# Performance work log

Hardware: AMD Instinct MI355X
Metric: run time of the kernel (lower is better)

The kernel has to match this reference:

```python
import jax, jax.numpy as jnp
import numpy as np

N, D, IN, OUT, K = 50000, 16, 256, 128, 4  # nodes, sampled degree, input_size, output_size, heads
LEAKY_SLOPE = 0.01  # torch F.leaky_relu default


def setup_inputs() -> dict:
    key = jax.random.key(0)
    k1, k2, k3, k4 = jax.random.split(key, 4)
    X = jax.random.normal(k1, (N, IN), dtype=jnp.float32)
    W = jax.random.normal(k2, (K, OUT, IN), dtype=jnp.float32) * 0.05
    a = jax.random.normal(k3, (K, 2 * OUT), dtype=jnp.float32) * 0.05
    neighbor_idx = jax.random.randint(k4, (N, D), 0, N)  # fixed-degree neighbor sample
    return {"X": X, "W": W, "a": a, "neighbor_idx": neighbor_idx}


def reference(X, W, a, neighbor_idx):
    # X: [N, IN]; W: [K, OUT, IN]; a: [K, 2*OUT]; neighbor_idx: [N, D]
    out_dim = W.shape[1]
    # Per-head linear map of every node once: Wh[k, n] = W[k] @ X[n]
    Wh = jnp.einsum('koi,ni->kno', W, X)                       # [K, N, OUT]
    # a splits: first OUT weights multiply mapped neighbour, second OUT multiply mapped self
    a_nb, a_self = a[:, :out_dim], a[:, out_dim:]
    e_nb = jnp.einsum('kno,ko->kn', Wh, a_nb)                  # [K, N] score contribution as a neighbour
    e_self = jnp.einsum('kno,ko->kn', Wh, a_self)              # [K, N] score contribution as center node
    # Edge logits: e[k, i, d] = leaky_relu(a_nb.Wh[j] + a_self.Wh[i]), j = neighbor_idx[i, d]
    e = jax.nn.leaky_relu(e_nb[:, neighbor_idx] + e_self[:, :, None], LEAKY_SLOPE)  # [K, N, D]
    alpha = jax.nn.softmax(e, axis=-1)                         # softmax over each node's neighbour set
    Wh_nb = jnp.take(Wh, neighbor_idx, axis=1)                 # [K, N, D, OUT] gathered neighbour features
    h = jnp.einsum('knd,kndo->kno', alpha, Wh_nb)              # [K, N, OUT] attention-weighted aggregate
    # Concatenate heads along feature dim, matching per-node head-concat in the torch loop
    return jnp.transpose(h, (1, 0, 2)).reshape(X.shape[0], -1)  # [N, K*OUT]
```

## Files before the change

### kernel.cpp

```cpp
#include <hip/hip_runtime.h>

#define N_NODES 50000
#define D_NB 16
#define IN_DIM 256
#define OUT_DIM 128
#define K_HEADS 4
#define SLOPE 0.01f
#define NSLICE 16
#define SLICE_COLS 32

typedef __attribute__((ext_vector_type(8))) short short8;
typedef __attribute__((ext_vector_type(4))) float f32x4;

static __device__ __forceinline__ unsigned f2bf(float f) {
    unsigned u = __float_as_uint(f);
    unsigned r = u + 0x7fffu + ((u >> 16) & 1u);
    return r >> 16;
}
static __device__ __forceinline__ float bf2f(unsigned short b) {
    return __uint_as_float(((unsigned)b) << 16);
}

__global__ void wb_kernel(const float* __restrict__ W, unsigned short* __restrict__ Wb) {
    int id = blockIdx.x * blockDim.x + threadIdx.x;
    if (id < K_HEADS * OUT_DIM * IN_DIM) Wb[id] = (unsigned short)f2bf(W[id]);
}

__global__ __launch_bounds__(256) void wt8_kernel(
    const float* __restrict__ W, const float* __restrict__ a, float* __restrict__ wt8)
{
    const int i = threadIdx.x;
    #pragma unroll
    for (int k = 0; k < K_HEADS; ++k) {
        float s0 = 0.f, s1 = 0.f;
        for (int o = 0; o < OUT_DIM; ++o) {
            const float w = W[((size_t)k * OUT_DIM + o) * IN_DIM + i];
            s0 += w * a[k * 2 * OUT_DIM + o];
            s1 += w * a[k * 2 * OUT_DIM + OUT_DIM + o];
        }
        wt8[(k * 2 + 0) * IN_DIM + i] = s0;
        wt8[(k * 2 + 1) * IN_DIM + i] = s1;
    }
}

__global__ __launch_bounds__(256) void prep_kernel(
    const float* __restrict__ X, const float* __restrict__ wt8,
    unsigned short* __restrict__ Xb, float* __restrict__ e_nb, float* __restrict__ e_self)
{
    const int t = threadIdx.x;
    const int w = t >> 6;
    const int lane = t & 63;
    const int n = blockIdx.x * 4 + w;

    const float4 x = *(const float4*)(X + (size_t)n * IN_DIM + lane * 4);
    uint2 pk;
    pk.x = f2bf(x.x) | (f2bf(x.y) << 16);
    pk.y = f2bf(x.z) | (f2bf(x.w) << 16);
    *(uint2*)(Xb + (size_t)n * IN_DIM + lane * 4) = pk;

    float p[8];
    #pragma unroll
    for (int v = 0; v < 8; ++v) {
        const float4 wv = *(const float4*)(wt8 + v * IN_DIM + lane * 4);
        p[v] = x.x * wv.x + x.y * wv.y + x.z * wv.z + x.w * wv.w;
    }
    #pragma unroll
    for (int sh = 32; sh >= 1; sh >>= 1) {
        #pragma unroll
        for (int v = 0; v < 8; ++v) p[v] += __shfl_xor(p[v], sh);
    }
    if (lane < 8) {
        const int k = lane >> 1;
        float* dst = (lane & 1) ? e_self : e_nb;
        dst[(size_t)k * N_NODES + n] = p[lane];
    }
}

__global__ __launch_bounds__(256) void agg_kernel(
    const int* __restrict__ nidx, const unsigned short* __restrict__ Xb,
    const float* __restrict__ e_nb, const float* __restrict__ e_self,
    unsigned short* __restrict__ aggX, int n0, int nc)
{
    const int t = threadIdx.x;
    const int w = t >> 6;
    const int lane = t & 63;
    const int n = n0 + blockIdx.x * 4 + w;
    if (n >= n0 + nc || n >= N_NODES) return;

    const int k = lane >> 4;
    const int dl = lane & 15;

    const int nbr = nidx[(size_t)n * D_NB + dl];
    const float x = e_nb[(size_t)k * N_NODES + nbr] + e_self[(size_t)k * N_NODES + n];
    const float v = x > 0.f ? x : SLOPE * x;
    float m = v;
    #pragma unroll
    for (int sh = 8; sh >= 1; sh >>= 1) m = fmaxf(m, __shfl_xor(m, sh, 16));
    const float pz = __expf(v - m);
    float sum = pz;
    #pragma unroll
    for (int sh = 8; sh >= 1; sh >>= 1) sum += __shfl_xor(sum, sh, 16);
    const float alpha = pz / sum;

    float acc[4][4] = {};
    #pragma unroll
    for (int h = 0; h < 2; ++h) {
        uint2 u[8];
        #pragma unroll
        for (int b = 0; b < 8; ++b) {
            const int nd = __shfl(nbr, h * 8 + b);
            u[b] = *(const uint2*)(Xb + (size_t)nd * IN_DIM + lane * 4);
        }
        #pragma unroll
        for (int b = 0; b < 8; ++b) {
            const float x0 = bf2f((unsigned short)(u[b].x & 0xffffu));
            const float x1 = bf2f((unsigned short)(u[b].x >> 16));
            const float x2 = bf2f((unsigned short)(u[b].y & 0xffffu));
            const float x3 = bf2f((unsigned short)(u[b].y >> 16));
            #pragma unroll
            for (int kk = 0; kk < 4; ++kk) {
                const float ad = __shfl(alpha, kk * 16 + h * 8 + b);
                acc[kk][0] += ad * x0;
                acc[kk][1] += ad * x1;
                acc[kk][2] += ad * x2;
                acc[kk][3] += ad * x3;
            }
        }
    }
    #pragma unroll
    for (int kk = 0; kk < 4; ++kk) {
        uint2 pk;
        pk.x = f2bf(acc[kk][0]) | (f2bf(acc[kk][1]) << 16);
        pk.y = f2bf(acc[kk][2]) | (f2bf(acc[kk][3]) << 16);
        *(uint2*)(aggX + ((size_t)kk * nc + (n - n0)) * IN_DIM + lane * 4) = pk;
    }
}

__global__ __launch_bounds__(256) void gemm2_kernel(
    const unsigned short* __restrict__ aggX, const unsigned short* __restrict__ Wb,
    float* __restrict__ out, int n0, int nc)
{
    __shared__ unsigned short Wlds[2][SLICE_COLS * IN_DIM];

    const int t = threadIdx.x;
    const int lane = t & 63;
    const int w = t >> 6;
    const int lrow = lane & 15;
    const int lk = lane >> 4;
    const int m0 = n0 + blockIdx.x * 64 + w * 16;

    const int arow = m0 + lrow;
    const bool avalid = (arow < n0 + nc) && (arow < N_NODES);

    auto STAGE = [&](int st, int buf) {
        const unsigned short* WbS = Wb + (size_t)st * SLICE_COLS * IN_DIM;
        #pragma unroll
        for (int i = 0; i < 4; ++i) {
            const int c = i * 256 + t;
            const int r = c >> 5;
            const int p = c & 31;
            const int cu = p ^ (r & 7);
            const unsigned short* gsrc = WbS + r * IN_DIM + cu * 8;
            unsigned short* ldst = &Wlds[buf][c * 8];
            __builtin_amdgcn_global_load_lds(
                (const __attribute__((address_space(1))) void*)gsrc,
                (__attribute__((address_space(3))) void*)ldst, 16, 0, 0);
        }
    };

    short8 af[8];
    STAGE(0, 0);
    __syncthreads();

    for (int st = 0; st < NSLICE; ++st) {
        const int buf = st & 1;
        if (st + 1 < NSLICE) STAGE(st + 1, buf ^ 1);

        if ((st & 3) == 0) {
            const unsigned short* Ar = aggX
                + ((size_t)(st >> 2) * nc + (arow - n0)) * IN_DIM + lk * 8;
            #pragma unroll
            for (int kk = 0; kk < 8; ++kk)
                af[kk] = avalid ? *(const short8*)(Ar + kk * 32)
                                : short8{0, 0, 0, 0, 0, 0, 0, 0};
        }

        f32x4 acc[2] = {};
        #pragma unroll
        for (int kk = 0; kk < 8; ++kk) {
            #pragma unroll
            for (int nt = 0; nt < 2; ++nt) {
                const int row = nt * 16 + lrow;
                const int pos = (kk * 4 + lk) ^ (row & 7);
                const short8 bf = *(const short8*)(&Wlds[buf][row * IN_DIM + pos * 8]);
                acc[nt] = __builtin_amdgcn_mfma_f32_16x16x32_bf16(bf, af[kk], acc[nt], 0, 0, 0);
            }
        }

        const int k = st >> 2, cb = st & 3;
        if (avalid) {
            #pragma unroll
            for (int nt = 0; nt < 2; ++nt) {
                *(f32x4*)(out + (size_t)arow * (K_HEADS * OUT_DIM)
                          + k * OUT_DIM + cb * SLICE_COLS + nt * 16 + lk * 4) = acc[nt];
            }
        }
        __syncthreads();
    }
}

extern "C" void kernel_launch(void* const* d_in, const int* in_sizes, int n_in,
                              void* d_out, int out_size, void* d_ws, size_t ws_size,
                              hipStream_t stream) {
    const float* X = (const float*)d_in[0];
    const float* W = (const float*)d_in[1];
    const float* a = (const float*)d_in[2];
    const int* nidx = (const int*)d_in[3];
    float* out = (float*)d_out;

    const size_t WbB  = (size_t)K_HEADS * OUT_DIM * IN_DIM * 2;
    const size_t XbB  = (size_t)N_NODES * IN_DIM * 2;
    const size_t wt8B = (size_t)8 * IN_DIM * 4;
    const size_t eB   = (size_t)K_HEADS * N_NODES * 4;
    auto need = [&](int nc) {
        return WbB + XbB + wt8B + 2 * eB + (size_t)K_HEADS * nc * IN_DIM * 2 + 1024;
    };

    int np, nc;
    if      (ws_size >= need(50000)) { np = 1; nc = 50000; }
    else if (ws_size >= need(25000)) { np = 2; nc = 25000; }
    else                             { np = 4; nc = 12500; }

    char* p = (char*)d_ws;
    unsigned short* Wb   = (unsigned short*)p;   p += WbB;
    unsigned short* Xb   = (unsigned short*)p;   p += XbB;
    float*          wt8  = (float*)p;            p += wt8B;
    float*          enb  = (float*)p;            p += eB;
    float*          esf  = (float*)p;            p += eB;
    unsigned short* aggX = (unsigned short*)p;

    hipLaunchKernelGGL(wb_kernel,
        dim3((K_HEADS * OUT_DIM * IN_DIM + 255) / 256), dim3(256), 0, stream, W, Wb);

    hipLaunchKernelGGL(wt8_kernel, dim3(1), dim3(256), 0, stream, W, a, wt8);

    hipLaunchKernelGGL(prep_kernel,
        dim3(N_NODES / 4), dim3(256), 0, stream, X, wt8, Xb, enb, esf);

    for (int pass = 0; pass < np; ++pass) {
        const int nb0 = pass * nc;
        hipLaunchKernelGGL(agg_kernel,
            dim3((nc + 3) / 4), dim3(256), 0, stream, nidx, Xb, enb, esf, aggX, nb0, nc);
        hipLaunchKernelGGL(gemm2_kernel,
            dim3((nc + 63) / 64), dim3(256), 0, stream, aggX, Wb, out, nb0, nc);
    }
}
```

Measured before the change: 177.1 us.

## Merge weight prep kernels, add nontemporal loads/stores, double GEMM block size

Merges the weight bf16 conversion kernel and the attention-vector projection kernel into one launch, which removes a kernel launch. Streaming input reads of X and the neighbour indices, and the output stores, now use nontemporal hints so they pollute the cache less. The GEMM kernel now uses 512 threads and 128 rows per block, so each LDS weight slice is shared by twice as many rows. The larger block may lower occupancy or tail efficiency.

```diff
diff --git a/kernel.cpp b/kernel.cpp
--- a/kernel.cpp
+++ b/kernel.cpp
@@ -11,6 +11,7 @@
 
 typedef __attribute__((ext_vector_type(8))) short short8;
 typedef __attribute__((ext_vector_type(4))) float f32x4;
+typedef __attribute__((ext_vector_type(2))) unsigned u32x2;
 
 static __device__ __forceinline__ unsigned f2bf(float f) {
     unsigned u = __float_as_uint(f);
@@ -21,14 +22,15 @@
     return __uint_as_float(((unsigned)b) << 16);
 }
 
-__global__ void wb_kernel(const float* __restrict__ W, unsigned short* __restrict__ Wb) {
-    int id = blockIdx.x * blockDim.x + threadIdx.x;
-    if (id < K_HEADS * OUT_DIM * IN_DIM) Wb[id] = (unsigned short)f2bf(W[id]);
-}
-
-__global__ __launch_bounds__(256) void wt8_kernel(
-    const float* __restrict__ W, const float* __restrict__ a, float* __restrict__ wt8)
-{
+__global__ __launch_bounds__(256) void prep_w_kernel(
+    const float* __restrict__ W, const float* __restrict__ a,
+    unsigned short* __restrict__ Wb, float* __restrict__ wt8)
+{
+    if (blockIdx.x < 2048) {
+        const int id = blockIdx.x * 256 + threadIdx.x;
+        Wb[id] = (unsigned short)f2bf(W[id]);
+        return;
+    }
     const int i = threadIdx.x;
     #pragma unroll
     for (int k = 0; k < K_HEADS; ++k) {
@@ -52,17 +54,18 @@
     const int lane = t & 63;
     const int n = blockIdx.x * 4 + w;
 
-    const float4 x = *(const float4*)(X + (size_t)n * IN_DIM + lane * 4);
+    const f32x4 x = __builtin_nontemporal_load(
+        (const f32x4*)(X + (size_t)n * IN_DIM + lane * 4));
     uint2 pk;
-    pk.x = f2bf(x.x) | (f2bf(x.y) << 16);
-    pk.y = f2bf(x.z) | (f2bf(x.w) << 16);
+    pk.x = f2bf(x[0]) | (f2bf(x[1]) << 16);
+    pk.y = f2bf(x[2]) | (f2bf(x[3]) << 16);
     *(uint2*)(Xb + (size_t)n * IN_DIM + lane * 4) = pk;
 
     float p[8];
     #pragma unroll
     for (int v = 0; v < 8; ++v) {
         const float4 wv = *(const float4*)(wt8 + v * IN_DIM + lane * 4);
-        p[v] = x.x * wv.x + x.y * wv.y + x.z * wv.z + x.w * wv.w;
+        p[v] = x[0] * wv.x + x[1] * wv.y + x[2] * wv.z + x[3] * wv.w;
     }
     #pragma unroll
     for (int sh = 32; sh >= 1; sh >>= 1) {
@@ -90,7 +93,7 @@
     const int k = lane >> 4;
     const int dl = lane & 15;
 
-    const int nbr = nidx[(size_t)n * D_NB + dl];
+    const int nbr = __builtin_nontemporal_load(nidx + (size_t)n * D_NB + dl);
     const float x = e_nb[(size_t)k * N_NODES + nbr] + e_self[(size_t)k * N_NODES + n];
     const float v = x > 0.f ? x : SLOPE * x;
     float m = v;
@@ -136,7 +139,7 @@
     }
 }
 
-__global__ __launch_bounds__(256) void gemm2_kernel(
+__global__ __launch_bounds__(512) void gemm2_kernel(
     const unsigned short* __restrict__ aggX, const unsigned short* __restrict__ Wb,
     float* __restrict__ out, int n0, int nc)
 {
@@ -147,7 +150,7 @@
     const int w = t >> 6;
     const int lrow = lane & 15;
     const int lk = lane >> 4;
-    const int m0 = n0 + blockIdx.x * 64 + w * 16;
+    const int m0 = n0 + blockIdx.x * 128 + w * 16;
 
     const int arow = m0 + lrow;
     const bool avalid = (arow < n0 + nc) && (arow < N_NODES);
@@ -155,8 +158,8 @@
     auto STAGE = [&](int st, int buf) {
         const unsigned short* WbS = Wb + (size_t)st * SLICE_COLS * IN_DIM;
         #pragma unroll
-        for (int i = 0; i < 4; ++i) {
-            const int c = i * 256 + t;
+        for (int i = 0; i < 2; ++i) {
+            const int c = i * 512 + t;
             const int r = c >> 5;
             const int p = c & 31;
             const int cu = p ^ (r & 7);
@@ -199,11 +202,11 @@
 
         const int k = st >> 2, cb = st & 3;
         if (avalid) {
-            #pragma unroll
-            for (int nt = 0; nt < 2; ++nt) {
-                *(f32x4*)(out + (size_t)arow * (K_HEADS * OUT_DIM)
-                          + k * OUT_DIM + cb * SLICE_COLS + nt * 16 + lk * 4) = acc[nt];
-            }
+            const size_t cbase = (size_t)arow * (K_HEADS * OUT_DIM)
+                               + (size_t)k * OUT_DIM + cb * SLICE_COLS + lk * 4;
+            #pragma unroll
+            for (int nt = 0; nt < 2; ++nt)
+                __builtin_nontemporal_store(acc[nt], (f32x4*)(out + cbase + nt * 16));
         }
         __syncthreads();
     }
@@ -239,10 +242,7 @@
     float*          esf  = (float*)p;            p += eB;
     unsigned short* aggX = (unsigned short*)p;
 
-    hipLaunchKernelGGL(wb_kernel,
-        dim3((K_HEADS * OUT_DIM * IN_DIM + 255) / 256), dim3(256), 0, stream, W, Wb);
-
-    hipLaunchKernelGGL(wt8_kernel, dim3(1), dim3(256), 0, stream, W, a, wt8);
+    hipLaunchKernelGGL(prep_w_kernel, dim3(2049), dim3(256), 0, stream, W, a, Wb, wt8);
 
     hipLaunchKernelGGL(prep_kernel,
         dim3(N_NODES / 4), dim3(256), 0, stream, X, wt8, Xb, enb, esf);
@@ -252,6 +252,6 @@
         hipLaunchKernelGGL(agg_kernel,
             dim3((nc + 3) / 4), dim3(256), 0, stream, nidx, Xb, enb, esf, aggX, nb0, nc);
         hipLaunchKernelGGL(gemm2_kernel,
-            dim3((nc + 63) / 64), dim3(256), 0, stream, aggX, Wb, out, nb0, nc);
-    }
-}
+            dim3((nc + 127) / 128), dim3(512), 0, stream, aggX, Wb, out, nb0, nc);
+    }
+}
```

After: 166.5 us. -5.9%, faster.
